# Performance work log

Hardware: AMD Instinct MI355X
Metric: run time of the kernel (lower is better)

Reference implementation:

```python
import jax, jax.numpy as jnp
import numpy as np

B, N, IN, HID, OUT = 64, 256, 7, 64, 32
DEG = 32
NT = B * N          # total nodes per side
E = NT * DEG        # intra-graph edges per side
TAU = 1.0
MAX_ITER = 10
EPS = 1e-5          # InstanceNorm2d eps


def setup_inputs() -> dict:
    key = jax.random.key(0)
    ks = jax.random.split(key, 12)

    def edges(k):
        # random intra-graph edges: local indices in [0, N) plus per-graph offset
        loc = jax.random.randint(k, (2, B, N * DEG), 0, N)
        off = (jnp.arange(B) * N)[None, :, None]
        return (loc + off).reshape(2, -1).astype(jnp.int64)

    def lin(k, fi, fo):
        return jax.random.normal(k, (fi, fo), jnp.float32) / np.float32(np.sqrt(fi))

    return {
        "x1": jax.random.normal(ks[0], (NT, IN), jnp.float32),
        "x2": jax.random.normal(ks[1], (NT, IN), jnp.float32),
        "edge1": edges(ks[2]),
        "edge2": edges(ks[3]),
        "Wl1": lin(ks[4], IN, HID), "Wr1": lin(ks[5], IN, HID),
        "bl1": jnp.zeros((HID,), jnp.float32), "br1": jnp.zeros((HID,), jnp.float32),
        "att1": jax.random.normal(ks[6], (HID,), jnp.float32) * 0.1,
        "bias1": jnp.zeros((HID,), jnp.float32),
        "Wl2": lin(ks[7], HID, OUT), "Wr2": lin(ks[8], HID, OUT),
        "bl2": jnp.zeros((OUT,), jnp.float32), "br2": jnp.zeros((OUT,), jnp.float32),
        "att2": jax.random.normal(ks[9], (OUT,), jnp.float32) * 0.1,
        "bias2": jnp.zeros((OUT,), jnp.float32),
        "gamma": jnp.ones((1,), jnp.float32),
        "beta": jnp.zeros((1,), jnp.float32),
    }


def _gatv2(x, src, dst, Wl, bl, Wr, br, att, bias):
    # PyG GATv2Conv, heads=1: score = att . leaky_relu(lin_l(x_j) + lin_r(x_i))
    xl = x @ Wl + bl  # source transform
    xr = x @ Wr + br  # target transform
    e = jax.nn.leaky_relu(xl[src] + xr[dst], 0.2)     # [E, D]
    score = e @ att                                    # [E]
    smax = jax.ops.segment_max(score, dst, num_segments=NT)
    ex = jnp.exp(score - smax[dst])
    den = jax.ops.segment_sum(ex, dst, num_segments=NT)
    alpha = ex / den[dst]
    out = jax.ops.segment_sum(alpha[:, None] * xl[src], dst, num_segments=NT)
    return out + bias


def _encode(x, edge, params):
    # add self loops (PyG add_self_loops=True default)
    loops = jnp.arange(NT)
    src = jnp.concatenate([edge[0], loops])
    dst = jnp.concatenate([edge[1], loops])
    h = jax.nn.relu(_gatv2(x, src, dst, *params[0]))
    return _gatv2(h, src, dst, *params[1])


def _soft_topk(sim_n):
    # AFAT-style differentiable top-k: OT between flattened scores and
    # {min, max} anchors with marginals [(n-k)/n, k/n], k = N2 per pair.
    n = N * N
    k = N
    flat = sim_n.reshape(B, n)
    mn = flat.min(axis=1, keepdims=True)
    mx = flat.max(axis=1, keepdims=True)
    dist = jnp.stack([flat - mn, mx - flat], axis=-1)  # [B, n, 2] (|s-min|,|s-max|)
    logK = -dist / TAU
    log_row = -jnp.log(jnp.float32(n))
    log_col = jnp.log(jnp.array([(n - k) / n, k / n], jnp.float32))
    for i in range(MAX_ITER):
        if i % 2 == 0:  # row normalization to uniform 1/n
            logK = logK - jax.scipy.special.logsumexp(logK, axis=-1, keepdims=True) + log_row
        else:           # column normalization to [(n-k)/n, k/n]
            logK = logK - jax.scipy.special.logsumexp(logK, axis=1, keepdims=True) + log_col[None, None, :]
    soft = jnp.clip(jnp.exp(logK[:, :, 1]) * n, 0.0, 1.0)  # selection probability per entry
    return soft.reshape(B, N, N)


def reference(x1, x2, edge1, edge2, Wl1, Wr1, bl1, br1, att1, bias1,
              Wl2, Wr2, bl2, br2, att2, bias2, gamma, beta):
    params = ((Wl1, bl1, Wr1, br1, att1, bias1), (Wl2, bl2, Wr2, br2, att2, bias2))
    h1 = _encode(x1, edge1, params).reshape(B, N, OUT)
    h2 = _encode(x2, edge2, params).reshape(B, N, OUT)
    sim = jnp.einsum('bnd,bmd->bnm', h1, h2)
    # InstanceNorm2d(1, affine=True): normalize each pair's sim matrix
    mu = sim.mean(axis=(1, 2), keepdims=True)
    var = sim.var(axis=(1, 2), keepdims=True)
    sim_n = gamma[0] * (sim - mu) * jax.lax.rsqrt(var + EPS) + beta[0]
    return _soft_topk(sim_n)  # soft_S stacked over the batch, [B, N, N]
```

## Files before the change

### kernel.cpp

```cpp
#include <hip/hip_runtime.h>

#define NB 64
#define NN 256
#define IND 7
#define HIDD 64
#define OUTD 32
#define EPG 8192
#define ETOT 524288
#define CAPQ 2600
#define SRCPAD 2624

typedef _Float16 f16;
typedef f16 f16x2 __attribute__((ext_vector_type(2)));
typedef f16 f16x4 __attribute__((ext_vector_type(4)));
typedef f16 f16x8 __attribute__((ext_vector_type(8)));
typedef float f32x4 __attribute__((ext_vector_type(4)));

__device__ __forceinline__ float bsum16(float v, float* rb){
#pragma unroll
  for (int o = 32; o > 0; o >>= 1) v += __shfl_xor(v, o, 64);
  __syncthreads();
  if ((threadIdx.x & 63) == 0) rb[threadIdx.x >> 6] = v;
  __syncthreads();
  float s = 0.f;
#pragma unroll
  for (int i = 0; i < 16; i++) s += rb[i];
  return s;
}
__device__ __forceinline__ float bmin16(float v, float* rb){
#pragma unroll
  for (int o = 32; o > 0; o >>= 1) v = fminf(v, __shfl_xor(v, o, 64));
  __syncthreads();
  if ((threadIdx.x & 63) == 0) rb[threadIdx.x >> 6] = v;
  __syncthreads();
  float s = rb[0];
#pragma unroll
  for (int i = 1; i < 16; i++) s = fminf(s, rb[i]);
  return s;
}
__device__ __forceinline__ float bmax16(float v, float* rb){
#pragma unroll
  for (int o = 32; o > 0; o >>= 1) v = fmaxf(v, __shfl_xor(v, o, 64));
  __syncthreads();
  if ((threadIdx.x & 63) == 0) rb[threadIdx.x >> 6] = v;
  __syncthreads();
  float s = rb[0];
#pragma unroll
  for (int i = 1; i < 16; i++) s = fmaxf(s, rb[i]);
  return s;
}

__device__ __forceinline__ f16x2 lrelu2(f16x2 s){
  const f16x2 k = {(f16)0.2f, (f16)0.2f};
  return __builtin_elementwise_max(s, s * k);
}
__device__ __forceinline__ f16x2 shfl_h2(f16x2 v, int lane){
  int i = __builtin_bit_cast(int, v);
  i = __shfl(i, lane, 64);
  return __builtin_bit_cast(f16x2, i);
}
__device__ __forceinline__ unsigned fkey(float f){
  unsigned b = __float_as_uint(f);
  return (b & 0x80000000u) ? ~b : (b | 0x80000000u);
}
__device__ __forceinline__ float fkinv(unsigned k){
  unsigned b = (k & 0x80000000u) ? (k ^ 0x80000000u) : ~k;
  return __uint_as_float(b);
}

__global__ __launch_bounds__(512, 4) void gat1(
    const float* __restrict__ x1, const float* __restrict__ x2,
    const int* __restrict__ e1, const int* __restrict__ e2,
    const float* __restrict__ Wl, const float* __restrict__ Wr,
    const float* __restrict__ bl, const float* __restrict__ br,
    const float* __restrict__ att, const float* __restrict__ bias,
    f16* __restrict__ hmid,
    int* __restrict__ meta, unsigned char* __restrict__ srcs,
    unsigned* __restrict__ stats)
{
  __shared__ __align__(16) f16 xl_s[256 * 72];
  __shared__ float sc_s[CAPQ];
  __shared__ unsigned int src_su[SRCPAD / 4];
  __shared__ int deg_s[64], start_s[64], cnt_s[64];
  __shared__ unsigned char perm[64];
  unsigned char* src_s = (unsigned char*)src_su;

  const int bid = blockIdx.x;
  const int gs = bid & 127, lo = (bid >> 7) * 64;
  const int side = gs >> 6, g = gs & 63;
  const float* x = side ? x2 : x1;
  const int* eb = side ? e2 : e1;
  const int* es = eb + g * EPG;
  const int* ed = eb + ETOT + g * EPG;
  const int t = threadIdx.x;

  if (bid == 0 && t < 256) stats[t] = ((t & 3) == 2) ? 0xFFFFFFFFu : 0u;

  if (t < 64) deg_s[t] = 0;

  unsigned short epk[17];
  int nE = 0;
#pragma unroll
  for (int i = 0; i < 17; i++){
    int e = t + i * 512;
    if (e < EPG + 256){
      int sl, dl;
      if (e < EPG){ sl = es[e] & 255; dl = ed[e] & 255; }
      else { sl = dl = e - EPG; }
      epk[i] = (unsigned short)((dl << 8) | sl);
      nE = i + 1;
    }
  }

  {
    const int node = t >> 1, dh = t & 1;
    float xv[IND];
    const float* xr_ = x + (g * 256 + node) * IND;
#pragma unroll
    for (int k = 0; k < IND; k++) xv[k] = xr_[k];
#pragma unroll
    for (int ch = 0; ch < 4; ch++){
      f16x8 o;
#pragma unroll
      for (int j = 0; j < 8; j++){
        int dd = dh * 32 + ch * 8 + j;
        float a = bl[dd];
#pragma unroll
        for (int k = 0; k < IND; k++) a = fmaf(xv[k], Wl[k * HIDD + dd], a);
        o[j] = (f16)a;
      }
      *(f16x8*)&xl_s[node * 72 + dh * 32 + ch * 8] = o;
    }
  }
  __syncthreads();

#pragma unroll
  for (int i = 0; i < 17; i++) if (i < nE){
    int r = (epk[i] >> 8) - lo;
    if ((unsigned)r < 64u) atomicAdd(&deg_s[r], 1);
  }
  __syncthreads();
  if (t < 64){
    int v = deg_s[t], s = v;
#pragma unroll
    for (int off = 1; off < 64; off <<= 1){
      int u = __shfl_up(s, off, 64);
      if (t >= off) s += u;
    }
    start_s[t] = s - v;
    cnt_s[t] = s - v;
    meta[bid * 128 + t] = s - v;
    meta[bid * 128 + 64 + t] = v;
    int r = 0;
#pragma unroll 8
    for (int j = 0; j < 64; j++){
      int dj = deg_s[j];
      r += (dj < v) || (dj == v && j < t);
    }
    perm[r] = (unsigned char)t;
  }
  __syncthreads();
#pragma unroll
  for (int i = 0; i < 17; i++) if (i < nE){
    int dl = epk[i] >> 8, r = dl - lo;
    if ((unsigned)r < 64u){
      int p = atomicAdd(&cnt_s[r], 1);
      if (p < CAPQ) src_s[p] = (unsigned char)(epk[i] & 255);
    }
  }
  __syncthreads();
  {
    int ttl = start_s[63] + deg_s[63];
    if (ttl > CAPQ) ttl = CAPQ;
    unsigned int* gsrc = (unsigned int*)(srcs + (size_t)bid * SRCPAD);
    int nw = (ttl + 3) >> 2;
    for (int i = t; i < nw; i += 512) gsrc[i] = src_su[i];
  }

  const int pairi = perm[t >> 3], sub = t & 7, ln = lo + pairi;
  f16x2 m[4], am[4];
  {
    float xv[IND];
    const float* xq = x + (g * 256 + ln) * IND;
#pragma unroll
    for (int k = 0; k < IND; k++) xv[k] = xq[k];
#pragma unroll
    for (int c = 0; c < 4; c++){
#pragma unroll
      for (int u = 0; u < 2; u++){
        int dd = sub * 8 + 2 * c + u;
        float a = br[dd];
#pragma unroll
        for (int k = 0; k < IND; k++) a = fmaf(xv[k], Wr[k * HIDD + dd], a);
        m[c][u] = (f16)a;
        am[c][u] = (f16)att[dd];
      }
    }
  }
  f16x2 xrh[32], atth[32];
  {
    const int base = (t & 63) & ~7;
#pragma unroll
    for (int ss = 0; ss < 8; ss++){
#pragma unroll
      for (int c = 0; c < 4; c++){
        xrh[ss * 4 + c] = shfl_h2(m[c], base + ss);
        atth[ss * 4 + c] = shfl_h2(am[c], base + ss);
      }
    }
  }

  const int s0 = start_s[pairi];
  int sE = s0 + deg_s[pairi];
  if (sE > CAPQ) sE = CAPQ;
  float ssum = 0.f;
  for (int idx = s0 + sub; idx < sE; idx += 8){
    int sl = src_s[idx];
    const f16x8* rp = (const f16x8*)&xl_s[(unsigned)sl * 72];
    float accs[4] = {0.f, 0.f, 0.f, 0.f};
#pragma unroll
    for (int blk = 0; blk < 8; blk++){
      f16x8 rv = rp[blk];
#pragma unroll
      for (int u = 0; u < 4; u++){
        f16x2 v = {rv[2 * u], rv[2 * u + 1]};
        v = v + xrh[blk * 4 + u];
        accs[u] = __builtin_amdgcn_fdot2(lrelu2(v), atth[blk * 4 + u], accs[u], false);
      }
    }
    float w = __expf((accs[0] + accs[1]) + (accs[2] + accs[3]));
    sc_s[idx] = w;
    ssum += w;
  }
  ssum += __shfl_xor(ssum, 1, 64);
  ssum += __shfl_xor(ssum, 2, 64);
  ssum += __shfl_xor(ssum, 4, 64);
  float inv = 1.f / ssum;
  float acc[8];
#pragma unroll
  for (int c = 0; c < 8; c++) acc[c] = 0.f;
  {
    int sl = (s0 < sE) ? src_s[s0] : 0;
    f16x8 row = *(const f16x8*)&xl_s[(unsigned)sl * 72 + sub * 8];
    for (int idx = s0; idx < sE; idx++){
      int sln = (idx + 1 < sE) ? src_s[idx + 1] : 0;
      f16x8 rown = *(const f16x8*)&xl_s[(unsigned)sln * 72 + sub * 8];
      float w = sc_s[idx];
#pragma unroll
      for (int c = 0; c < 8; c++) acc[c] = fmaf(w, (float)row[c], acc[c]);
      row = rown;
    }
  }
  f16x8 o;
#pragma unroll
  for (int c = 0; c < 8; c++)
    o[c] = (f16)fmaxf(acc[c] * inv + bias[sub * 8 + c], 0.f);
  *(f16x8*)(hmid + (size_t)(gs * 256 + ln) * 64 + sub * 8) = o;
}

__global__ __launch_bounds__(512, 4) void gat2(
    const int* __restrict__ meta, const unsigned char* __restrict__ srcs,
    const f16* __restrict__ hmid,
    const float* __restrict__ Wl, const float* __restrict__ Wr,
    const float* __restrict__ bl, const float* __restrict__ br,
    const float* __restrict__ att, const float* __restrict__ bias,
    f16* __restrict__ hout)
{
  __shared__ __align__(16) f16 xl_s[256 * 40];
  __shared__ __align__(16) f16 xr_s[64 * 40];
  __shared__ float sc_s[CAPQ];
  __shared__ unsigned int src_su[SRCPAD / 4];
  __shared__ int start_s[64], deg_s[64];
  __shared__ unsigned char perm[64];
  unsigned char* src_s = (unsigned char*)src_su;

  const int bid = blockIdx.x;
  const int gs = bid & 127, lo = (bid >> 7) * 64;
  const int t = threadIdx.x;

  if (t < 64){
    start_s[t] = meta[bid * 128 + t];
    deg_s[t] = meta[bid * 128 + 64 + t];
  }
  {
    int ttl = meta[bid * 128 + 63] + meta[bid * 128 + 64 + 63];
    if (ttl > CAPQ) ttl = CAPQ;
    const unsigned int* gsrc = (const unsigned int*)(srcs + (size_t)bid * SRCPAD);
    int nw = (ttl + 3) >> 2;
    for (int i = t; i < nw; i += 512) src_su[i] = gsrc[i];
  }

  {
    const int w = t >> 6, lane = t & 63;
    const int m = lane & 15, quad = lane >> 4;
    f16x8 a[2][2];
#pragma unroll
    for (int ti = 0; ti < 2; ti++){
      const f16* arow = hmid + (size_t)(gs * 256 + (2 * w + ti) * 16 + m) * 64;
      a[ti][0] = *(const f16x8*)(arow + quad * 8);
      a[ti][1] = *(const f16x8*)(arow + 32 + quad * 8);
    }
#pragma unroll
    for (int H = 0; H < 2; H++){
      const int n = H * 16 + m;
      f16x8 b0, b1;
#pragma unroll
      for (int j = 0; j < 8; j++){
        b0[j] = (f16)Wl[(quad * 8 + j) * 32 + n];
        b1[j] = (f16)Wl[(32 + quad * 8 + j) * 32 + n];
      }
      const float bv = bl[n];
#pragma unroll
      for (int ti = 0; ti < 2; ti++){
        f32x4 acc = {0.f, 0.f, 0.f, 0.f};
        acc = __builtin_amdgcn_mfma_f32_16x16x32_f16(a[ti][0], b0, acc, 0, 0, 0);
        acc = __builtin_amdgcn_mfma_f32_16x16x32_f16(a[ti][1], b1, acc, 0, 0, 0);
#pragma unroll
        for (int r = 0; r < 4; r++)
          xl_s[((2 * w + ti) * 16 + quad * 4 + r) * 40 + n] = (f16)(acc[r] + bv);
      }
    }
    if (w < 4){
      const f16* arow = hmid + (size_t)(gs * 256 + lo + w * 16 + m) * 64;
      f16x8 c0 = *(const f16x8*)(arow + quad * 8);
      f16x8 c1 = *(const f16x8*)(arow + 32 + quad * 8);
#pragma unroll
      for (int H = 0; H < 2; H++){
        const int n = H * 16 + m;
        f16x8 b0, b1;
#pragma unroll
        for (int j = 0; j < 8; j++){
          b0[j] = (f16)Wr[(quad * 8 + j) * 32 + n];
          b1[j] = (f16)Wr[(32 + quad * 8 + j) * 32 + n];
        }
        const float bv = br[n];
        f32x4 acc = {0.f, 0.f, 0.f, 0.f};
        acc = __builtin_amdgcn_mfma_f32_16x16x32_f16(c0, b0, acc, 0, 0, 0);
        acc = __builtin_amdgcn_mfma_f32_16x16x32_f16(c1, b1, acc, 0, 0, 0);
#pragma unroll
        for (int r = 0; r < 4; r++)
          xr_s[(w * 16 + quad * 4 + r) * 40 + n] = (f16)(acc[r] + bv);
      }
    }
  }
  __syncthreads();
  if (t < 64){
    int v = deg_s[t], r = 0;
#pragma unroll 8
    for (int j = 0; j < 64; j++){
      int dj = deg_s[j];
      r += (dj < v) || (dj == v && j < t);
    }
    perm[r] = (unsigned char)t;
  }
  __syncthreads();

  const int pairi = perm[t >> 3], sub = t & 7, ln = lo + pairi;
  f16x2 xrh[16], atth[16];
  {
    const f16x8* xrp = (const f16x8*)&xr_s[pairi * 40];
#pragma unroll
    for (int q = 0; q < 4; q++){
      f16x8 v = xrp[q];
#pragma unroll
      for (int u = 0; u < 4; u++){
        xrh[q * 4 + u][0] = v[2 * u];
        xrh[q * 4 + u][1] = v[2 * u + 1];
      }
    }
#pragma unroll
    for (int i = 0; i < 16; i++){
      atth[i][0] = (f16)att[2 * i];
      atth[i][1] = (f16)att[2 * i + 1];
    }
  }

  const int s0 = start_s[pairi];
  int sE = s0 + deg_s[pairi];
  if (sE > CAPQ) sE = CAPQ;
  float ssum = 0.f;
  for (int idx = s0 + sub; idx < sE; idx += 8){
    int sl = src_s[idx];
    const f16x8* rp = (const f16x8*)&xl_s[(unsigned)sl * 40];
    float accs[4] = {0.f, 0.f, 0.f, 0.f};
#pragma unroll
    for (int blk = 0; blk < 4; blk++){
      f16x8 rv = rp[blk];
#pragma unroll
      for (int u = 0; u < 4; u++){
        f16x2 v = {rv[2 * u], rv[2 * u + 1]};
        v = v + xrh[blk * 4 + u];
        accs[u] = __builtin_amdgcn_fdot2(lrelu2(v), atth[blk * 4 + u], accs[u], false);
      }
    }
    float w = __expf((accs[0] + accs[1]) + (accs[2] + accs[3]));
    sc_s[idx] = w;
    ssum += w;
  }
  ssum += __shfl_xor(ssum, 1, 64);
  ssum += __shfl_xor(ssum, 2, 64);
  ssum += __shfl_xor(ssum, 4, 64);
  float inv = 1.f / ssum;

  float acc[4];
#pragma unroll
  for (int c = 0; c < 4; c++) acc[c] = 0.f;
  {
    int sl = (s0 < sE) ? src_s[s0] : 0;
    f16x4 row = *(const f16x4*)&xl_s[(unsigned)sl * 40 + sub * 4];
    for (int idx = s0; idx < sE; idx++){
      int sln = (idx + 1 < sE) ? src_s[idx + 1] : 0;
      f16x4 rown = *(const f16x4*)&xl_s[(unsigned)sln * 40 + sub * 4];
      float w = sc_s[idx];
#pragma unroll
      for (int c = 0; c < 4; c++) acc[c] = fmaf(w, (float)row[c], acc[c]);
      row = rown;
    }
  }
  f16x4 o;
#pragma unroll
  for (int c = 0; c < 4; c++)
    o[c] = (f16)(acc[c] * inv + bias[sub * 4 + c]);
  *(f16x4*)(hout + (size_t)(gs * 256 + ln) * 32 + sub * 4) = o;
}

__global__ __launch_bounds__(1024) void simk(
    const f16* __restrict__ H, f16* __restrict__ simh,
    unsigned* __restrict__ stats)
{
  __shared__ float rb[16];
  const int b = blockIdx.x & 63, q = blockIdx.x >> 6, t = threadIdx.x;
  const int w = t >> 6, lane = t & 63;
  const int m = lane & 15, quad = lane >> 4;
  const int rowT = q * 64 + (w & 3) * 16;
  const int colB = (w >> 2) * 64;

  const f16* h1 = H + (size_t)b * 256 * 32;
  const f16* h2 = H + (size_t)(64 + b) * 256 * 32;

  f16x8 av = *(const f16x8*)(h1 + (size_t)(rowT + m) * 32 + quad * 8);
  f32x4 c[4];
#pragma unroll
  for (int jj = 0; jj < 4; jj++){
    f16x8 bv = *(const f16x8*)(h2 + (size_t)(colB + jj * 16 + m) * 32 + quad * 8);
    f32x4 z = {0.f, 0.f, 0.f, 0.f};
    c[jj] = __builtin_amdgcn_mfma_f32_16x16x32_f16(av, bv, z, 0, 0, 0);
  }

  float sm = 0.f, s2 = 0.f, mn = 3.0e38f, mx = -3.0e38f;
  f16* ob = simh + (size_t)b * 65536;
#pragma unroll
  for (int jj = 0; jj < 4; jj++)
#pragma unroll
    for (int r = 0; r < 4; r++){
      float s = c[jj][r];
      sm += s; s2 = fmaf(s, s, s2);
      mn = fminf(mn, s); mx = fmaxf(mx, s);
      ob[(rowT + quad * 4 + r) * 256 + colB + jj * 16 + m] = (f16)s;
    }
  sm = bsum16(sm, rb);
  s2 = bsum16(s2, rb);
  mn = bmin16(mn, rb);
  mx = bmax16(mx, rb);
  if (t == 0){
    atomicAdd((float*)&stats[b * 4 + 0], sm);
    atomicAdd((float*)&stats[b * 4 + 1], s2);
    atomicMin(&stats[b * 4 + 2], fkey(mn));
    atomicMax(&stats[b * 4 + 3], fkey(mx));
  }
}

__global__ __launch_bounds__(1024) void sinkk(
    const f16* __restrict__ simh, const unsigned* __restrict__ stats,
    const float* __restrict__ gamma, const float* __restrict__ beta,
    float* __restrict__ res)
{
  __shared__ float rb[16];
  __shared__ unsigned int hist[8192];
  const int b = blockIdx.x, t = threadIdx.x;

  const float sum = __uint_as_float(stats[b * 4 + 0]);
  const float ssq = __uint_as_float(stats[b * 4 + 1]);
  const float mn = fkinv(stats[b * 4 + 2]);
  const float mx = fkinv(stats[b * 4 + 3]);

  const float mu = sum * (1.f / 65536.f);
  const float var = ssq * (1.f / 65536.f) - mu * mu;
  const float a = gamma[0] * rsqrtf(var + 1e-5f);
  const float cc = beta[0] - a * mu;
  float mnn = a * mn + cc, mxn = a * mx + cc;
  if (a < 0.f){ float tmp = mnn; mnn = mxn; mxn = tmp; }
  const float al = 2.f * a;
  const float be = 2.f * cc - mnn - mxn;
  const float R = fmaxf(mxn - mnn, 1e-12f);
  const float binscale = 4096.f / R;

  for (int i = t; i < 8192; i += 1024) hist[i] = 0u;
  __syncthreads();
  const f16x8* sp = (const f16x8*)(simh + (size_t)b * 65536);
#pragma unroll
  for (int ch = 0; ch < 8; ch++){
    f16x8 v = sp[ch * 1024 + t];
#pragma unroll
    for (int u = 0; u < 8; u++){
      float z = fmaf(al, (float)v[u], be);
      int bi = (int)fmaf(z, binscale, 4096.f);
      bi = min(max(bi, 0), 8191);
      atomicAdd(&hist[bi], 1u);
    }
  }
  __syncthreads();

  const float wbin = R * (1.f / 4096.f);
  float ebs[8], cnts[8];
#pragma unroll
  for (int j = 0; j < 8; j++){
    float zc = fmaf((float)(t * 8 + j) + 0.5f, wbin, -R);
    ebs[j] = __expf(-zc);
    cnts[j] = (float)hist[t * 8 + j];
  }

  float D = 0.f, S = 256.f, eD = 1.f;
  for (int p = 0; p < 5; p++){
    float loc = 0.f;
#pragma unroll
    for (int j = 0; j < 8; j++)
      loc += cnts[j] / (1.f + ebs[j] * eD);
    S = bsum16(loc, rb);
    if (p < 4){
      D += -5.5412635f  + __logf(65536.f - S) - __logf(S);
      eD = __expf(-D);
    }
  }
  if (t == 0){
    res[b * 4 + 0] = al;
    res[b * 4 + 1] = be + D;
    res[b * 4 + 2] = 256.f / S;
  }
}

__global__ __launch_bounds__(256) void outk(
    const f16* __restrict__ simh, const float* __restrict__ res,
    float* __restrict__ out)
{
  const int b = blockIdx.x & 63, seg = blockIdx.x >> 6, t = threadIdx.x;
  const float al = res[b * 4 + 0];
  const float beD = res[b * 4 + 1];
  const float scale = res[b * 4 + 2];
  const f16x8* sp = (const f16x8*)(simh + (size_t)b * 65536 + seg * 8192);
  f32x4* ob = (f32x4*)(out + (size_t)b * 65536 + seg * 8192);
#pragma unroll
  for (int k = 0; k < 4; k++){
    f16x8 v = sp[k * 256 + t];
    f32x4 o0, o1;
#pragma unroll
    for (int u = 0; u < 4; u++){
      float z0 = fmaf(al, (float)v[u], beD);
      float z1 = fmaf(al, (float)v[4 + u], beD);
      o0[u] = fminf(scale / (1.f + __expf(-z0)), 1.f);
      o1[u] = fminf(scale / (1.f + __expf(-z1)), 1.f);
    }
    ob[(k * 256 + t) * 2] = o0;
    ob[(k * 256 + t) * 2 + 1] = o1;
  }
}

extern "C" void kernel_launch(void* const* d_in, const int* in_sizes, int n_in,
                              void* d_out, int out_size, void* d_ws, size_t ws_size,
                              hipStream_t stream)
{
  const float* x1   = (const float*)d_in[0];
  const float* x2   = (const float*)d_in[1];
  const int*   e1   = (const int*)d_in[2];
  const int*   e2   = (const int*)d_in[3];
  const float* Wl1  = (const float*)d_in[4];
  const float* Wr1  = (const float*)d_in[5];
  const float* bl1  = (const float*)d_in[6];
  const float* br1  = (const float*)d_in[7];
  const float* att1 = (const float*)d_in[8];
  const float* bias1= (const float*)d_in[9];
  const float* Wl2  = (const float*)d_in[10];
  const float* Wr2  = (const float*)d_in[11];
  const float* bl2  = (const float*)d_in[12];
  const float* br2  = (const float*)d_in[13];
  const float* att2 = (const float*)d_in[14];
  const float* bias2= (const float*)d_in[15];
  const float* gamma= (const float*)d_in[16];
  const float* beta = (const float*)d_in[17];

  char* ws = (char*)d_ws;
  f16* hfin = (f16*)ws;
  f16* hmid = (f16*)(ws + (size_t)2 * 1024 * 1024);
  int* meta = (int*)(ws + (size_t)6 * 1024 * 1024);
  unsigned char* srcs = (unsigned char*)(ws + (size_t)6 * 1024 * 1024 + 512 * 128 * 4);
  f16* simh = (f16*)(ws + (size_t)2 * 1024 * 1024);
  unsigned* stats = (unsigned*)(ws + (size_t)10 * 1024 * 1024);
  float* res = (float*)(ws + (size_t)10 * 1024 * 1024 + 4096);
  float* out = (float*)d_out;

  gat1<<<512, 512, 0, stream>>>(x1, x2, e1, e2, Wl1, Wr1, bl1, br1, att1, bias1,
                                hmid, meta, srcs, stats);
  gat2<<<512, 512, 0, stream>>>(meta, srcs, hmid, Wl2, Wr2, bl2, br2, att2, bias2, hfin);
  simk<<<256, 1024, 0, stream>>>(hfin, simh, stats);
  sinkk<<<64, 1024, 0, stream>>>(simh, stats, gamma, beta, res);
  outk<<<512, 256, 0, stream>>>(simh, res, out);
}
```

Measured before the change: 181.4 us.

## Recompute similarity matrix in sinkhorn and output kernels instead of storing it

Removes the separate similarity kernel and its fp16 intermediate buffer plus global atomics for statistics. The sinkhorn kernel now computes each batch's full 256x256 similarity with MFMA in registers, reduces mean/var/min/max in-block, and builds the histogram directly. The output kernel recomputes the similarity tile via MFMA and applies the sigmoid scaling. This trades a small amount of redundant matmul work for less global memory traffic and one fewer launch, but sinkk now does more work per block with only 64 blocks.

```diff
diff --git a/kernel.cpp b/kernel.cpp
--- a/kernel.cpp
+++ b/kernel.cpp
@@ -59,14 +59,6 @@
   i = __shfl(i, lane, 64);
   return __builtin_bit_cast(f16x2, i);
 }
-__device__ __forceinline__ unsigned fkey(float f){
-  unsigned b = __float_as_uint(f);
-  return (b & 0x80000000u) ? ~b : (b | 0x80000000u);
-}
-__device__ __forceinline__ float fkinv(unsigned k){
-  unsigned b = (k & 0x80000000u) ? (k ^ 0x80000000u) : ~k;
-  return __uint_as_float(b);
-}
 
 __global__ __launch_bounds__(512, 4) void gat1(
     const float* __restrict__ x1, const float* __restrict__ x2,
@@ -75,8 +67,7 @@
     const float* __restrict__ bl, const float* __restrict__ br,
     const float* __restrict__ att, const float* __restrict__ bias,
     f16* __restrict__ hmid,
-    int* __restrict__ meta, unsigned char* __restrict__ srcs,
-    unsigned* __restrict__ stats)
+    int* __restrict__ meta, unsigned char* __restrict__ srcs)
 {
   __shared__ __align__(16) f16 xl_s[256 * 72];
   __shared__ float sc_s[CAPQ];
@@ -93,8 +84,6 @@
   const int* es = eb + g * EPG;
   const int* ed = eb + ETOT + g * EPG;
   const int t = threadIdx.x;
-
-  if (bid == 0 && t < 256) stats[t] = ((t & 3) == 2) ? 0xFFFFFFFFu : 0u;
 
   if (t < 64) deg_s[t] = 0;
 
@@ -424,68 +413,45 @@
   *(f16x4*)(hout + (size_t)(gs * 256 + ln) * 32 + sub * 4) = o;
 }
 
-__global__ __launch_bounds__(1024) void simk(
-    const f16* __restrict__ H, f16* __restrict__ simh,
-    unsigned* __restrict__ stats)
-{
-  __shared__ float rb[16];
-  const int b = blockIdx.x & 63, q = blockIdx.x >> 6, t = threadIdx.x;
-  const int w = t >> 6, lane = t & 63;
-  const int m = lane & 15, quad = lane >> 4;
-  const int rowT = q * 64 + (w & 3) * 16;
-  const int colB = (w >> 2) * 64;
-
-  const f16* h1 = H + (size_t)b * 256 * 32;
-  const f16* h2 = H + (size_t)(64 + b) * 256 * 32;
-
-  f16x8 av = *(const f16x8*)(h1 + (size_t)(rowT + m) * 32 + quad * 8);
-  f32x4 c[4];
-#pragma unroll
-  for (int jj = 0; jj < 4; jj++){
-    f16x8 bv = *(const f16x8*)(h2 + (size_t)(colB + jj * 16 + m) * 32 + quad * 8);
-    f32x4 z = {0.f, 0.f, 0.f, 0.f};
-    c[jj] = __builtin_amdgcn_mfma_f32_16x16x32_f16(av, bv, z, 0, 0, 0);
-  }
-
-  float sm = 0.f, s2 = 0.f, mn = 3.0e38f, mx = -3.0e38f;
-  f16* ob = simh + (size_t)b * 65536;
-#pragma unroll
-  for (int jj = 0; jj < 4; jj++)
-#pragma unroll
-    for (int r = 0; r < 4; r++){
-      float s = c[jj][r];
-      sm += s; s2 = fmaf(s, s, s2);
-      mn = fminf(mn, s); mx = fmaxf(mx, s);
-      ob[(rowT + quad * 4 + r) * 256 + colB + jj * 16 + m] = (f16)s;
-    }
-  sm = bsum16(sm, rb);
-  s2 = bsum16(s2, rb);
-  mn = bmin16(mn, rb);
-  mx = bmax16(mx, rb);
-  if (t == 0){
-    atomicAdd((float*)&stats[b * 4 + 0], sm);
-    atomicAdd((float*)&stats[b * 4 + 1], s2);
-    atomicMin(&stats[b * 4 + 2], fkey(mn));
-    atomicMax(&stats[b * 4 + 3], fkey(mx));
-  }
-}
-
 __global__ __launch_bounds__(1024) void sinkk(
-    const f16* __restrict__ simh, const unsigned* __restrict__ stats,
+    const f16* __restrict__ H,
     const float* __restrict__ gamma, const float* __restrict__ beta,
     float* __restrict__ res)
 {
   __shared__ float rb[16];
   __shared__ unsigned int hist[8192];
   const int b = blockIdx.x, t = threadIdx.x;
-
-  const float sum = __uint_as_float(stats[b * 4 + 0]);
-  const float ssq = __uint_as_float(stats[b * 4 + 1]);
-  const float mn = fkinv(stats[b * 4 + 2]);
-  const float mx = fkinv(stats[b * 4 + 3]);
-
-  const float mu = sum * (1.f / 65536.f);
-  const float var = ssq * (1.f / 65536.f) - mu * mu;
+  const int w = t >> 6, lane = t & 63;
+  const int m = lane & 15, quad = lane >> 4;
+
+  const f16* h1 = H + (size_t)b * 256 * 32;
+  const f16* h2 = H + (size_t)(64 + b) * 256 * 32;
+
+  f16x8 av = *(const f16x8*)(h1 + (size_t)(w * 16 + m) * 32 + quad * 8);
+  f32x4 c[16];
+#pragma unroll
+  for (int j = 0; j < 16; j++){
+    f16x8 bv = *(const f16x8*)(h2 + (size_t)(j * 16 + m) * 32 + quad * 8);
+    f32x4 z = {0.f, 0.f, 0.f, 0.f};
+    c[j] = __builtin_amdgcn_mfma_f32_16x16x32_f16(av, bv, z, 0, 0, 0);
+  }
+
+  float sm = 0.f, s2 = 0.f, mn = 3.0e38f, mx = -3.0e38f;
+#pragma unroll
+  for (int j = 0; j < 16; j++)
+#pragma unroll
+    for (int r = 0; r < 4; r++){
+      float s = c[j][r];
+      sm += s; s2 = fmaf(s, s, s2);
+      mn = fminf(mn, s); mx = fmaxf(mx, s);
+    }
+  sm = bsum16(sm, rb);
+  s2 = bsum16(s2, rb);
+  mn = bmin16(mn, rb);
+  mx = bmax16(mx, rb);
+
+  const float mu = sm * (1.f / 65536.f);
+  const float var = s2 * (1.f / 65536.f) - mu * mu;
   const float a = gamma[0] * rsqrtf(var + 1e-5f);
   const float cc = beta[0] - a * mu;
   float mnn = a * mn + cc, mxn = a * mx + cc;
@@ -497,18 +463,15 @@
 
   for (int i = t; i < 8192; i += 1024) hist[i] = 0u;
   __syncthreads();
-  const f16x8* sp = (const f16x8*)(simh + (size_t)b * 65536);
-#pragma unroll
-  for (int ch = 0; ch < 8; ch++){
-    f16x8 v = sp[ch * 1024 + t];
-#pragma unroll
-    for (int u = 0; u < 8; u++){
-      float z = fmaf(al, (float)v[u], be);
+#pragma unroll
+  for (int j = 0; j < 16; j++)
+#pragma unroll
+    for (int r = 0; r < 4; r++){
+      float z = fmaf(al, c[j][r], be);
       int bi = (int)fmaf(z, binscale, 4096.f);
       bi = min(max(bi, 0), 8191);
       atomicAdd(&hist[bi], 1u);
     }
-  }
   __syncthreads();
 
   const float wbin = R * (1.f / 4096.f);
@@ -539,29 +502,36 @@
   }
 }
 
-__global__ __launch_bounds__(256) void outk(
-    const f16* __restrict__ simh, const float* __restrict__ res,
+__global__ __launch_bounds__(1024) void outk(
+    const f16* __restrict__ H, const float* __restrict__ res,
     float* __restrict__ out)
 {
-  const int b = blockIdx.x & 63, seg = blockIdx.x >> 6, t = threadIdx.x;
+  const int b = blockIdx.x & 63, q = blockIdx.x >> 6, t = threadIdx.x;
+  const int w = t >> 6, lane = t & 63;
+  const int m = lane & 15, quad = lane >> 4;
+  const int rowT = q * 64 + (w & 3) * 16;
+  const int colB = (w >> 2) * 64;
+
   const float al = res[b * 4 + 0];
   const float beD = res[b * 4 + 1];
   const float scale = res[b * 4 + 2];
-  const f16x8* sp = (const f16x8*)(simh + (size_t)b * 65536 + seg * 8192);
-  f32x4* ob = (f32x4*)(out + (size_t)b * 65536 + seg * 8192);
-#pragma unroll
-  for (int k = 0; k < 4; k++){
-    f16x8 v = sp[k * 256 + t];
-    f32x4 o0, o1;
-#pragma unroll
-    for (int u = 0; u < 4; u++){
-      float z0 = fmaf(al, (float)v[u], beD);
-      float z1 = fmaf(al, (float)v[4 + u], beD);
-      o0[u] = fminf(scale / (1.f + __expf(-z0)), 1.f);
-      o1[u] = fminf(scale / (1.f + __expf(-z1)), 1.f);
-    }
-    ob[(k * 256 + t) * 2] = o0;
-    ob[(k * 256 + t) * 2 + 1] = o1;
+
+  const f16* h1 = H + (size_t)b * 256 * 32;
+  const f16* h2 = H + (size_t)(64 + b) * 256 * 32;
+
+  f16x8 av = *(const f16x8*)(h1 + (size_t)(rowT + m) * 32 + quad * 8);
+  float* ob = out + (size_t)b * 65536;
+#pragma unroll
+  for (int jj = 0; jj < 4; jj++){
+    f16x8 bv = *(const f16x8*)(h2 + (size_t)(colB + jj * 16 + m) * 32 + quad * 8);
+    f32x4 z = {0.f, 0.f, 0.f, 0.f};
+    f32x4 c = __builtin_amdgcn_mfma_f32_16x16x32_f16(av, bv, z, 0, 0, 0);
+#pragma unroll
+    for (int r = 0; r < 4; r++){
+      float zz = fmaf(al, c[r], beD);
+      float v = fminf(scale / (1.f + __expf(-zz)), 1.f);
+      ob[(rowT + quad * 4 + r) * 256 + colB + jj * 16 + m] = v;
+    }
   }
 }
 
@@ -593,15 +563,12 @@
   f16* hmid = (f16*)(ws + (size_t)2 * 1024 * 1024);
   int* meta = (int*)(ws + (size_t)6 * 1024 * 1024);
   unsigned char* srcs = (unsigned char*)(ws + (size_t)6 * 1024 * 1024 + 512 * 128 * 4);
-  f16* simh = (f16*)(ws + (size_t)2 * 1024 * 1024);
-  unsigned* stats = (unsigned*)(ws + (size_t)10 * 1024 * 1024);
-  float* res = (float*)(ws + (size_t)10 * 1024 * 1024 + 4096);
+  float* res = (float*)(ws + (size_t)8 * 1024 * 1024);
   float* out = (float*)d_out;
 
   gat1<<<512, 512, 0, stream>>>(x1, x2, e1, e2, Wl1, Wr1, bl1, br1, att1, bias1,
-                                hmid, meta, srcs, stats);
+                                hmid, meta, srcs);
   gat2<<<512, 512, 0, stream>>>(meta, srcs, hmid, Wl2, Wr2, bl2, br2, att2, bias2, hfin);
-  simk<<<256, 1024, 0, stream>>>(hfin, simh, stats);
-  sinkk<<<64, 1024, 0, stream>>>(simh, stats, gamma, beta, res);
-  outk<<<512, 256, 0, stream>>>(simh, res, out);
-}
+  sinkk<<<64, 1024, 0, stream>>>(hfin, gamma, beta, res);
+  outk<<<256, 1024, 0, stream>>>(hfin, res, out);
+}
```

After: 177.0 us. -2.4%, faster.
